# Kernel optimization log

Measured on AMD Instinct MI355X. Metric: run time of the kernel, lower is better.

## Reference

```python
import jax, jax.numpy as jnp
import numpy as np

D_MODEL = 1024
HEADS = 16
D_K = D_MODEL // HEADS
NEG_INF = -1e10


def setup_inputs() -> dict:
    key = jax.random.key(0)
    ks = jax.random.split(key, 10)
    n, s = 2, 2048
    inp = {
        "value": jax.random.normal(ks[0], (n, s, D_MODEL), dtype=jnp.float32),
        "key": jax.random.normal(ks[1], (n, s, D_MODEL), dtype=jnp.float32),
        "query": jax.random.normal(ks[2], (n, s, D_MODEL), dtype=jnp.float32),
        "mask": jax.random.randint(ks[3], (n, 1, s, s), 0, 2, dtype=jnp.int32),
        # torch.nn.Linear weights are [out, in]; y = x @ W.T (+ b)
        "Wq": jax.random.normal(ks[4], (D_MODEL, D_MODEL), dtype=jnp.float32) * (D_MODEL ** -0.5),
        "Wk": jax.random.normal(ks[5], (D_MODEL, D_MODEL), dtype=jnp.float32) * (D_MODEL ** -0.5),
        "Wv": jax.random.normal(ks[6], (D_MODEL, D_MODEL), dtype=jnp.float32) * (D_MODEL ** -0.5),
        "Wo": jax.random.normal(ks[7], (D_MODEL, D_MODEL), dtype=jnp.float32) * (D_MODEL ** -0.5),
        "bo": jax.random.normal(ks[8], (D_MODEL,), dtype=jnp.float32) * 0.01,
    }
    return inp


def reference(value, key, query, mask, Wq, Wk, Wv, Wo, bo):
    n, q_len, _ = query.shape
    # projections (Linear, no bias): x @ W.T
    q = (query @ Wq.T).reshape(n, q_len, HEADS, D_K)
    k = (key @ Wk.T).reshape(n, key.shape[1], HEADS, D_K)
    v = (value @ Wv.T).reshape(n, value.shape[1], HEADS, D_K)
    scores = jnp.einsum('nqhd,nkhd->nhqk', q, k)  # [n,h,q,k]
    scores = jnp.where(mask == 0, jnp.float32(NEG_INF), scores)
    attn = jax.nn.softmax(scores / jnp.sqrt(jnp.float32(D_K)), axis=-1)
    out = jnp.einsum('nhql,nlhd->nqhd', attn, v).reshape(n, q_len, D_MODEL)
    return out @ Wo.T + bo
```

## Files before the change

### kernel.cpp

```cpp
#include <hip/hip_runtime.h>
#include <hip/hip_bf16.h>
#include <stdint.h>

#define SEQ     2048
#define NBATCH  2
#define DMODEL  1024
#define NH      16
#define DKH     64

typedef __bf16 bf16;
typedef __attribute__((ext_vector_type(8))) __bf16 bf16x8;
typedef __attribute__((ext_vector_type(4))) __bf16 bf16x4;
typedef __attribute__((ext_vector_type(4))) float  f32x4;

static __device__ __forceinline__ f32x4 mfma16(bf16x8 a, bf16x8 b, f32x4 c) {
    return __builtin_amdgcn_mfma_f32_16x16x32_bf16(a, b, c, 0, 0, 0);
}

typedef const __attribute__((address_space(1))) void* gas_cptr;
typedef __attribute__((address_space(3))) void*       las_ptr;
#define GLDS16(g, l) __builtin_amdgcn_global_load_lds((gas_cptr)(g), (las_ptr)(l), 16, 0, 0)

#define PL32SWAP(a, b) asm("v_permlane32_swap_b32 %0, %1" : "+v"(a), "+v"(b))
#define PL16SWAP(a, b) asm("v_permlane16_swap_b32 %0, %1" : "+v"(a), "+v"(b))

__global__ __launch_bounds__(256) void cvt_all_k(const float* __restrict__ q,
                                                 const float* __restrict__ k,
                                                 const float* __restrict__ v,
                                                 const float* __restrict__ wq,
                                                 const float* __restrict__ wk,
                                                 const float* __restrict__ wv,
                                                 const float* __restrict__ wo,
                                                 const int* __restrict__ mask,
                                                 bf16* __restrict__ qb, bf16* __restrict__ kb,
                                                 bf16* __restrict__ vb, bf16* __restrict__ wqb,
                                                 bf16* __restrict__ wkb, bf16* __restrict__ wvb,
                                                 bf16* __restrict__ wob,
                                                 unsigned long long* __restrict__ mbits) {
    if (blockIdx.y == 7) {
        const int nwords = NBATCH * SEQ * (SEQ / 64);
        int wave  = (blockIdx.x * blockDim.x + threadIdx.x) >> 6;
        int lane  = threadIdx.x & 63;
        int nwtot = (gridDim.x * blockDim.x) >> 6;
        for (int w = wave; w < nwords; w += nwtot) {
            int m = mask[(size_t)w * 64 + lane];
            unsigned long long b = __ballot(m != 0);
            if (lane == 0) mbits[w] = b;
        }
        return;
    }
    const float* src; bf16* dst; int n4;
    const int NX4 = (NBATCH * SEQ * DMODEL) / 4, NW4 = (DMODEL * DMODEL) / 4;
    switch (blockIdx.y) {
        case 0: src = q;  dst = qb;  n4 = NX4; break;
        case 1: src = k;  dst = kb;  n4 = NX4; break;
        case 2: src = v;  dst = vb;  n4 = NX4; break;
        case 3: src = wq; dst = wqb; n4 = NW4; break;
        case 4: src = wk; dst = wkb; n4 = NW4; break;
        case 5: src = wv; dst = wvb; n4 = NW4; break;
        default: src = wo; dst = wob; n4 = NW4; break;
    }
    int stride = gridDim.x * blockDim.x;
    for (int i = blockIdx.x * blockDim.x + threadIdx.x; i < n4; i += stride) {
        f32x4 f = ((const f32x4*)src)[i];
        bf16x4 o;
#pragma unroll
        for (int j = 0; j < 4; j++) o[j] = (bf16)f[j];
        ((bf16x4*)dst)[i] = o;
    }
}

__global__ __launch_bounds__(256) void qkv_gemm(const bf16* __restrict__ Xq,
                                                const bf16* __restrict__ Xk,
                                                const bf16* __restrict__ Xv,
                                                const bf16* __restrict__ Wq,
                                                const bf16* __restrict__ Wk,
                                                const bf16* __restrict__ Wv,
                                                bf16* __restrict__ Qo,
                                                bf16* __restrict__ Ko,
                                                bf16* __restrict__ Vto) {
    __shared__ bf16 As[128 * 32], Bs[128 * 32];
    const int z = blockIdx.z;
    const bf16* A = (z == 0) ? Xq : (z == 1) ? Xk : Xv;
    const bf16* W = (z == 0) ? Wq : (z == 1) ? Wk : Wv;
    const int bm = blockIdx.x * 128, bn = blockIdx.y * 128;
    const int tid = threadIdx.x, wave = tid >> 6, lane = tid & 63;
    const int wm = wave >> 1, wn = wave & 1, lo = lane & 15, hi = lane >> 4;

    const int r0 = wave * 32 + (lane >> 2);
    const int c8 = (lane & 3) * 8;
    const bf16* Ag = A + (size_t)(bm + r0) * DMODEL + c8;
    const bf16* Bg = W + (size_t)(bn + r0) * DMODEL + c8;
    bf16* lA = &As[wave * 1024];
    bf16* lB = &Bs[wave * 1024];

    f32x4 acc[4][4];
#pragma unroll
    for (int i = 0; i < 4; i++)
#pragma unroll
        for (int j = 0; j < 4; j++) acc[i][j] = 0.0f;

    for (int k0 = 0; k0 < DMODEL; k0 += 32) {
        __syncthreads();
        GLDS16(Ag + k0, lA);
        GLDS16(Ag + k0 + (size_t)16 * DMODEL, lA + 512);
        GLDS16(Bg + k0, lB);
        GLDS16(Bg + k0 + (size_t)16 * DMODEL, lB + 512);
        __syncthreads();

        bf16x8 a[4], b[4];
#pragma unroll
        for (int t = 0; t < 4; t++) {
            a[t] = *(const bf16x8*)&As[(wm * 64 + t * 16 + lo) * 32 + hi * 8];
            b[t] = *(const bf16x8*)&Bs[(wn * 64 + t * 16 + lo) * 32 + hi * 8];
        }
#pragma unroll
        for (int tm = 0; tm < 4; tm++)
#pragma unroll
            for (int tn = 0; tn < 4; tn++)
                acc[tm][tn] = mfma16(a[tm], b[tn], acc[tm][tn]);
    }

    if (z < 2) {
        bf16* O = (z == 0) ? Qo : Ko;
        const float qscale = (z == 0) ? 0.18033688f : 1.0f;
#pragma unroll
        for (int tm = 0; tm < 4; tm++)
#pragma unroll
            for (int tn = 0; tn < 4; tn++)
#pragma unroll
                for (int r = 0; r < 4; r++) {
                    int m = bm + wm * 64 + tm * 16 + hi * 4 + r;
                    int o = bn + wn * 64 + tn * 16 + lo;
                    int nidx = m >> 11, sq = m & 2047;
                    int hh = o >> 6, d = o & 63;
                    O[(((size_t)nidx * NH + hh) * SEQ + sq) * DKH + d] = (bf16)(acc[tm][tn][r] * qscale);
                }
    } else {
#pragma unroll
        for (int tm = 0; tm < 4; tm++)
#pragma unroll
            for (int tn = 0; tn < 4; tn++)
#pragma unroll
                for (int r = 0; r < 4; r++) {
                    int m = bm + wm * 64 + tm * 16 + hi * 4 + r;
                    int o = bn + wn * 64 + tn * 16 + lo;
                    int nidx = m >> 11, sq = m & 2047;
                    int hh = o >> 6, d = o & 63;
                    Vto[(((size_t)nidx * NH + hh) * DKH + d) * SEQ + sq] = (bf16)acc[tm][tn][r];
                }
    }
}

__global__ __launch_bounds__(256, 8) void attn_k(const bf16* __restrict__ Q,
                                                 const bf16* __restrict__ K,
                                                 const bf16* __restrict__ Vt,
                                                 const unsigned long long* __restrict__ mbits,
                                                 bf16* __restrict__ Op0,
                                                 bf16* __restrict__ Op1,
                                                 float* __restrict__ Lp) {
    __shared__ bf16 Ks[64 * 72];
    __shared__ bf16 Vs[64 * 72];

    const int bid = blockIdx.x;
    const int xcd = bid & 7, j = bid >> 3;
    const int hd = xcd * 4 + (j & 3);
    const int qb = (j >> 2) & 31;
    const int ks = j >> 7;
    const int n = hd >> 4, h = hd & 15;

    const int tid = threadIdx.x, wave = tid >> 6, lane = tid & 63;
    const int lo = lane & 15, hi = lane >> 4;

    const size_t headoff = (size_t)hd * SEQ * DKH;
    const bf16* Qh = Q + headoff;
    const bf16* Kh = K + headoff;
    const bf16* Vh = Vt + headoff;

    const int qrow = qb * 64 + wave * 16 + lo;
    const bf16x8 aq0 = *(const bf16x8*)(Qh + (size_t)qrow * DKH + hi * 8);
    const bf16x8 aq1 = *(const bf16x8*)(Qh + (size_t)qrow * DKH + 32 + hi * 8);

    bf16x8 ones;
#pragma unroll
    for (int i = 0; i < 8; i++) ones[i] = (bf16)1.0f;

    f32x4 oacc[4];
#pragma unroll
    for (int t = 0; t < 4; t++) oacc[t] = 0.0f;
    f32x4 lacc; lacc = 0.0f;

    const unsigned long long* mbq = mbits + ((size_t)n * SEQ + qrow) * (SEQ / 64);

    const int kbeg = ks * 1024, kend = kbeg + 1024;

    const int srow = tid >> 3, sseg = tid & 7;
    const bf16* Kg = Kh + (size_t)srow * DKH + sseg * 8;
    const bf16* Vg = Vh + (size_t)srow * SEQ + sseg * 8;

    bf16x8 rk0 = *(const bf16x8*)(Kg + (size_t)kbeg * DKH);
    bf16x8 rk1 = *(const bf16x8*)(Kg + (size_t)(kbeg + 32) * DKH);
    bf16x8 rv0 = *(const bf16x8*)(Vg + kbeg);
    bf16x8 rv1 = *(const bf16x8*)(Vg + (size_t)32 * SEQ + kbeg);
    unsigned long long wm = mbq[kbeg >> 6];
    unsigned long long wmn = 0;

#pragma unroll 1
    for (int k0 = kbeg; k0 < kend; k0 += 64) {
        __syncthreads();
        *(bf16x8*)&Ks[srow * 72 + sseg * 8]        = rk0;
        *(bf16x8*)&Ks[(srow + 32) * 72 + sseg * 8] = rk1;
        *(bf16x8*)&Vs[srow * 72 + sseg * 8]        = rv0;
        *(bf16x8*)&Vs[(srow + 32) * 72 + sseg * 8] = rv1;
        if (k0 + 64 < kend) {
            rk0 = *(const bf16x8*)(Kg + (size_t)(k0 + 64) * DKH);
            rk1 = *(const bf16x8*)(Kg + (size_t)(k0 + 96) * DKH);
            rv0 = *(const bf16x8*)(Vg + k0 + 64);
            rv1 = *(const bf16x8*)(Vg + (size_t)32 * SEQ + k0 + 64);
            wmn = mbq[(k0 >> 6) + 1];
        }
        __syncthreads();

        unsigned wlo = (unsigned)(wm >> (hi * 4));
        unsigned whi = (unsigned)(wm >> (hi * 4 + 32));
        uint32_t pk[4][2];
#pragma unroll
        for (int tn = 0; tn < 4; tn++) {
            const int kr = (tn * 16 + lo) * 72;
            bf16x8 b0 = *(const bf16x8*)&Ks[kr + hi * 8];
            bf16x8 b1 = *(const bf16x8*)&Ks[kr + 32 + hi * 8];
            f32x4 z4; z4 = 0.0f;
            z4 = mfma16(b0, aq0, z4);
            z4 = mfma16(b1, aq1, z4);
            unsigned ws = ((tn < 2) ? wlo : whi) >> ((tn & 1) * 16);
            float pv[4];
#pragma unroll
            for (int r = 0; r < 4; r++) {
                float e = __builtin_amdgcn_exp2f(z4[r]);
                pv[r] = ((ws >> r) & 1u) ? e : 0.0f;
            }
            asm("v_cvt_pk_bf16_f32 %0, %1, %2" : "=v"(pk[tn][0]) : "v"(pv[0]), "v"(pv[1]));
            asm("v_cvt_pk_bf16_f32 %0, %1, %2" : "=v"(pk[tn][1]) : "v"(pv[2]), "v"(pv[3]));
        }
        wm = wmn;

        uint32_t d00 = pk[0][0], d02 = pk[1][0];
        PL32SWAP(d00, d02); PL16SWAP(d00, d02);
        uint32_t d01 = pk[0][1], d03 = pk[1][1];
        PL32SWAP(d01, d03); PL16SWAP(d01, d03);
        uint32_t d10 = pk[2][0], d12 = pk[3][0];
        PL32SWAP(d10, d12); PL16SWAP(d10, d12);
        uint32_t d11 = pk[2][1], d13 = pk[3][1];
        PL32SWAP(d11, d13); PL16SWAP(d11, d13);

        union FragU { uint32_t u[4]; bf16x8 v; };
        FragU f0, f1;
        f0.u[0] = d00; f0.u[1] = d01; f0.u[2] = d02; f0.u[3] = d03;
        f1.u[0] = d10; f1.u[1] = d11; f1.u[2] = d12; f1.u[3] = d13;
        bf16x8 ap0 = f0.v;
        bf16x8 ap1 = f1.v;

#pragma unroll
        for (int td = 0; td < 4; td++) {
            bf16x8 b0 = *(const bf16x8*)&Vs[(td * 16 + lo) * 72 + hi * 8];
            bf16x8 b1 = *(const bf16x8*)&Vs[(td * 16 + lo) * 72 + 32 + hi * 8];
            oacc[td] = mfma16(ap0, b0, oacc[td]);
            oacc[td] = mfma16(ap1, b1, oacc[td]);
        }
        lacc = mfma16(ap0, ones, lacc);
        lacc = mfma16(ap1, ones, lacc);
    }

    bf16* Op = ks ? Op1 : Op0;
#pragma unroll
    for (int td = 0; td < 4; td++)
#pragma unroll
        for (int r = 0; r < 4; r++) {
            int q = qb * 64 + wave * 16 + hi * 4 + r;
            int d = td * 16 + lo;
            Op[((size_t)n * SEQ + q) * DMODEL + h * 64 + d] = (bf16)oacc[td][r];
        }
    if (lo == 0) {
#pragma unroll
        for (int r = 0; r < 4; r++) {
            int q = qb * 64 + wave * 16 + hi * 4 + r;
            Lp[(size_t)ks * (NBATCH * NH * SEQ) + ((size_t)(n * NH + h) * SEQ) + q] = lacc[r];
        }
    }
}

__global__ __launch_bounds__(256) void merge_k(const bf16* __restrict__ o0,
                                               const bf16* __restrict__ o1,
                                               const float* __restrict__ lp,
                                               bf16* __restrict__ Aout) {
    int t = blockIdx.x * blockDim.x + threadIdx.x;
    int q = t >> 7;
    int h = (t >> 3) & 15;
    int n = q >> 11;
    bf16x8 a = ((const bf16x8*)o0)[t];
    bf16x8 b = ((const bf16x8*)o1)[t];
    int li = (n * NH + h) * SEQ + (q & 2047);
    float l = lp[li] + lp[NBATCH * NH * SEQ + li];
    float rl = 1.0f / l;
    bf16x8 o;
#pragma unroll
    for (int i = 0; i < 8; i++) o[i] = (bf16)(((float)a[i] + (float)b[i]) * rl);
    ((bf16x8*)Aout)[t] = o;
}

__global__ __launch_bounds__(256) void out_gemm(const bf16* __restrict__ A,
                                                const bf16* __restrict__ W,
                                                const float* __restrict__ bias,
                                                float* __restrict__ Out) {
    __shared__ bf16 As[128 * 32], Bs[128 * 32];
    const int bm = blockIdx.x * 128, bn = blockIdx.y * 128;
    const int tid = threadIdx.x, wave = tid >> 6, lane = tid & 63;
    const int wm = wave >> 1, wn = wave & 1, lo = lane & 15, hi = lane >> 4;

    const int r0 = wave * 32 + (lane >> 2);
    const int c8 = (lane & 3) * 8;
    const bf16* Ag = A + (size_t)(bm + r0) * DMODEL + c8;
    const bf16* Bg = W + (size_t)(bn + r0) * DMODEL + c8;
    bf16* lA = &As[wave * 1024];
    bf16* lB = &Bs[wave * 1024];

    f32x4 acc[4][4];
#pragma unroll
    for (int i = 0; i < 4; i++)
#pragma unroll
        for (int j = 0; j < 4; j++) acc[i][j] = 0.0f;

    for (int k0 = 0; k0 < DMODEL; k0 += 32) {
        __syncthreads();
        GLDS16(Ag + k0, lA);
        GLDS16(Ag + k0 + (size_t)16 * DMODEL, lA + 512);
        GLDS16(Bg + k0, lB);
        GLDS16(Bg + k0 + (size_t)16 * DMODEL, lB + 512);
        __syncthreads();

        bf16x8 a[4], b[4];
#pragma unroll
        for (int t = 0; t < 4; t++) {
            a[t] = *(const bf16x8*)&As[(wm * 64 + t * 16 + lo) * 32 + hi * 8];
            b[t] = *(const bf16x8*)&Bs[(wn * 64 + t * 16 + lo) * 32 + hi * 8];
        }
#pragma unroll
        for (int tm = 0; tm < 4; tm++)
#pragma unroll
            for (int tn = 0; tn < 4; tn++)
                acc[tm][tn] = mfma16(a[tm], b[tn], acc[tm][tn]);
    }

#pragma unroll
    for (int tm = 0; tm < 4; tm++)
#pragma unroll
        for (int tn = 0; tn < 4; tn++) {
            int o = bn + wn * 64 + tn * 16 + lo;
            float bv = bias[o];
#pragma unroll
            for (int r = 0; r < 4; r++) {
                int m = bm + wm * 64 + tm * 16 + hi * 4 + r;
                Out[(size_t)m * DMODEL + o] = acc[tm][tn][r] + bv;
            }
        }
}

extern "C" void kernel_launch(void* const* d_in, const int* in_sizes, int n_in,
                              void* d_out, int out_size, void* d_ws, size_t ws_size,
                              hipStream_t stream) {
    const float* value = (const float*)d_in[0];
    const float* key   = (const float*)d_in[1];
    const float* query = (const float*)d_in[2];
    const int*   mask  = (const int*)d_in[3];
    const float* Wq    = (const float*)d_in[4];
    const float* Wk    = (const float*)d_in[5];
    const float* Wv    = (const float*)d_in[6];
    const float* Wo    = (const float*)d_in[7];
    const float* bo    = (const float*)d_in[8];
    float* out = (float*)d_out;

    char* ws = (char*)d_ws;
    bf16* Qws = (bf16*)(ws);
    bf16* Kws = (bf16*)(ws + (8u  << 20));
    bf16* Vt  = (bf16*)(ws + (16u << 20));
    bf16* Xqb = (bf16*)(ws + (24u << 20));
    bf16* Xkb = (bf16*)(ws + (32u << 20));
    bf16* Xvb = (bf16*)(ws + (40u << 20));
    bf16* Wqb = (bf16*)(ws + (48u << 20));
    bf16* Wkb = (bf16*)(ws + (50u << 20));
    bf16* Wvb = (bf16*)(ws + (52u << 20));
    bf16* Wob = (bf16*)(ws + (54u << 20));
    unsigned long long* mbits = (unsigned long long*)(ws + (56u << 20));
    bf16*  Op0 = Xqb;
    bf16*  Op1 = Xkb;
    bf16*  Aws = Xvb;
    float* Lp  = (float*)Wqb;

    cvt_all_k<<<dim3(1024, 8), 256, 0, stream>>>(query, key, value, Wq, Wk, Wv, Wo, mask,
                                                 Xqb, Xkb, Xvb, Wqb, Wkb, Wvb, Wob, mbits);
    qkv_gemm<<<dim3(32, 8, 3), 256, 0, stream>>>(Xqb, Xkb, Xvb, Wqb, Wkb, Wvb, Qws, Kws, Vt);
    attn_k<<<2048, 256, 0, stream>>>(Qws, Kws, Vt, mbits, Op0, Op1, Lp);
    merge_k<<<2048, 256, 0, stream>>>(Op0, Op1, Lp, Aws);
    out_gemm<<<dim3(32, 8), 256, 0, stream>>>(Aws, Wob, bo, out);
}
```

Measured before the change: 331.0 us.

## Process two query tiles per attention block to reuse staged K/V tiles

Each attention block now handles 128 query rows (two 64-row sub-tiles) instead of 64, so every K/V tile staged in shared memory feeds twice as many MFMAs. The grid is halved to 1024 blocks and the occupancy hint drops from 8 to 4 blocks per CU to make room for the doubled accumulators and Q fragments. This cuts global K/V traffic and per-tile sync overhead, at the cost of higher register pressure and fewer resident waves to hide latency.

```diff
diff --git a/kernel.cpp b/kernel.cpp
--- a/kernel.cpp
+++ b/kernel.cpp
@@ -152,7 +152,7 @@
     }
 }
 
-__global__ __launch_bounds__(256, 8) void attn_k(const bf16* __restrict__ Q,
+__global__ __launch_bounds__(256, 4) void attn_k(const bf16* __restrict__ Q,
                                                  const bf16* __restrict__ K,
                                                  const bf16* __restrict__ Vt,
                                                  const unsigned long long* __restrict__ mbits,
@@ -165,8 +165,8 @@
     const int bid = blockIdx.x;
     const int xcd = bid & 7, j = bid >> 3;
     const int hd = xcd * 4 + (j & 3);
-    const int qb = (j >> 2) & 31;
-    const int ks = j >> 7;
+    const int qb = (j >> 2) & 15;
+    const int ks = j >> 6;
     const int n = hd >> 4, h = hd & 15;
 
     const int tid = threadIdx.x, wave = tid >> 6, lane = tid & 63;
@@ -177,20 +177,25 @@
     const bf16* Kh = K + headoff;
     const bf16* Vh = Vt + headoff;
 
-    const int qrow = qb * 64 + wave * 16 + lo;
-    const bf16x8 aq0 = *(const bf16x8*)(Qh + (size_t)qrow * DKH + hi * 8);
-    const bf16x8 aq1 = *(const bf16x8*)(Qh + (size_t)qrow * DKH + 32 + hi * 8);
+    const int qrowA = qb * 128 + wave * 16 + lo;
+    const int qrowB = qrowA + 64;
+    const bf16x8 aq0A = *(const bf16x8*)(Qh + (size_t)qrowA * DKH + hi * 8);
+    const bf16x8 aq1A = *(const bf16x8*)(Qh + (size_t)qrowA * DKH + 32 + hi * 8);
+    const bf16x8 aq0B = *(const bf16x8*)(Qh + (size_t)qrowB * DKH + hi * 8);
+    const bf16x8 aq1B = *(const bf16x8*)(Qh + (size_t)qrowB * DKH + 32 + hi * 8);
 
     bf16x8 ones;
 #pragma unroll
     for (int i = 0; i < 8; i++) ones[i] = (bf16)1.0f;
 
-    f32x4 oacc[4];
-#pragma unroll
-    for (int t = 0; t < 4; t++) oacc[t] = 0.0f;
-    f32x4 lacc; lacc = 0.0f;
-
-    const unsigned long long* mbq = mbits + ((size_t)n * SEQ + qrow) * (SEQ / 64);
+    f32x4 oaccA[4], oaccB[4];
+#pragma unroll
+    for (int t = 0; t < 4; t++) { oaccA[t] = 0.0f; oaccB[t] = 0.0f; }
+    f32x4 laccA; laccA = 0.0f;
+    f32x4 laccB; laccB = 0.0f;
+
+    const unsigned long long* mbqA = mbits + ((size_t)n * SEQ + qrowA) * (SEQ / 64);
+    const unsigned long long* mbqB = mbits + ((size_t)n * SEQ + qrowB) * (SEQ / 64);
 
     const int kbeg = ks * 1024, kend = kbeg + 1024;
 
@@ -202,8 +207,11 @@
     bf16x8 rk1 = *(const bf16x8*)(Kg + (size_t)(kbeg + 32) * DKH);
     bf16x8 rv0 = *(const bf16x8*)(Vg + kbeg);
     bf16x8 rv1 = *(const bf16x8*)(Vg + (size_t)32 * SEQ + kbeg);
-    unsigned long long wm = mbq[kbeg >> 6];
-    unsigned long long wmn = 0;
+    unsigned long long wmA = mbqA[kbeg >> 6];
+    unsigned long long wmB = mbqB[kbeg >> 6];
+    unsigned long long wmnA = 0, wmnB = 0;
+
+    union FragU { uint32_t u[4]; bf16x8 v; };
 
 #pragma unroll 1
     for (int k0 = kbeg; k0 < kend; k0 += 64) {
@@ -217,58 +225,88 @@
             rk1 = *(const bf16x8*)(Kg + (size_t)(k0 + 96) * DKH);
             rv0 = *(const bf16x8*)(Vg + k0 + 64);
             rv1 = *(const bf16x8*)(Vg + (size_t)32 * SEQ + k0 + 64);
-            wmn = mbq[(k0 >> 6) + 1];
-        }
-        __syncthreads();
-
-        unsigned wlo = (unsigned)(wm >> (hi * 4));
-        unsigned whi = (unsigned)(wm >> (hi * 4 + 32));
-        uint32_t pk[4][2];
+            wmnA = mbqA[(k0 >> 6) + 1];
+            wmnB = mbqB[(k0 >> 6) + 1];
+        }
+        __syncthreads();
+
+        unsigned wloA = (unsigned)(wmA >> (hi * 4));
+        unsigned whiA = (unsigned)(wmA >> (hi * 4 + 32));
+        unsigned wloB = (unsigned)(wmB >> (hi * 4));
+        unsigned whiB = (unsigned)(wmB >> (hi * 4 + 32));
+        uint32_t pkA[4][2], pkB[4][2];
 #pragma unroll
         for (int tn = 0; tn < 4; tn++) {
             const int kr = (tn * 16 + lo) * 72;
             bf16x8 b0 = *(const bf16x8*)&Ks[kr + hi * 8];
             bf16x8 b1 = *(const bf16x8*)&Ks[kr + 32 + hi * 8];
-            f32x4 z4; z4 = 0.0f;
-            z4 = mfma16(b0, aq0, z4);
-            z4 = mfma16(b1, aq1, z4);
-            unsigned ws = ((tn < 2) ? wlo : whi) >> ((tn & 1) * 16);
-            float pv[4];
+            f32x4 zA; zA = 0.0f;
+            zA = mfma16(b0, aq0A, zA);
+            zA = mfma16(b1, aq1A, zA);
+            f32x4 zB; zB = 0.0f;
+            zB = mfma16(b0, aq0B, zB);
+            zB = mfma16(b1, aq1B, zB);
+            unsigned wsA = ((tn < 2) ? wloA : whiA) >> ((tn & 1) * 16);
+            unsigned wsB = ((tn < 2) ? wloB : whiB) >> ((tn & 1) * 16);
+            float pvA[4], pvB[4];
 #pragma unroll
             for (int r = 0; r < 4; r++) {
-                float e = __builtin_amdgcn_exp2f(z4[r]);
-                pv[r] = ((ws >> r) & 1u) ? e : 0.0f;
+                float eA = __builtin_amdgcn_exp2f(zA[r]);
+                pvA[r] = ((wsA >> r) & 1u) ? eA : 0.0f;
+                float eB = __builtin_amdgcn_exp2f(zB[r]);
+                pvB[r] = ((wsB >> r) & 1u) ? eB : 0.0f;
             }
-            asm("v_cvt_pk_bf16_f32 %0, %1, %2" : "=v"(pk[tn][0]) : "v"(pv[0]), "v"(pv[1]));
-            asm("v_cvt_pk_bf16_f32 %0, %1, %2" : "=v"(pk[tn][1]) : "v"(pv[2]), "v"(pv[3]));
-        }
-        wm = wmn;
-
-        uint32_t d00 = pk[0][0], d02 = pk[1][0];
-        PL32SWAP(d00, d02); PL16SWAP(d00, d02);
-        uint32_t d01 = pk[0][1], d03 = pk[1][1];
-        PL32SWAP(d01, d03); PL16SWAP(d01, d03);
-        uint32_t d10 = pk[2][0], d12 = pk[3][0];
-        PL32SWAP(d10, d12); PL16SWAP(d10, d12);
-        uint32_t d11 = pk[2][1], d13 = pk[3][1];
-        PL32SWAP(d11, d13); PL16SWAP(d11, d13);
-
-        union FragU { uint32_t u[4]; bf16x8 v; };
-        FragU f0, f1;
-        f0.u[0] = d00; f0.u[1] = d01; f0.u[2] = d02; f0.u[3] = d03;
-        f1.u[0] = d10; f1.u[1] = d11; f1.u[2] = d12; f1.u[3] = d13;
-        bf16x8 ap0 = f0.v;
-        bf16x8 ap1 = f1.v;
+            asm("v_cvt_pk_bf16_f32 %0, %1, %2" : "=v"(pkA[tn][0]) : "v"(pvA[0]), "v"(pvA[1]));
+            asm("v_cvt_pk_bf16_f32 %0, %1, %2" : "=v"(pkA[tn][1]) : "v"(pvA[2]), "v"(pvA[3]));
+            asm("v_cvt_pk_bf16_f32 %0, %1, %2" : "=v"(pkB[tn][0]) : "v"(pvB[0]), "v"(pvB[1]));
+            asm("v_cvt_pk_bf16_f32 %0, %1, %2" : "=v"(pkB[tn][1]) : "v"(pvB[2]), "v"(pvB[3]));
+        }
+        wmA = wmnA;
+        wmB = wmnB;
+
+        bf16x8 ap0A, ap1A, ap0B, ap1B;
+        {
+            uint32_t d00 = pkA[0][0], d02 = pkA[1][0];
+            PL32SWAP(d00, d02); PL16SWAP(d00, d02);
+            uint32_t d01 = pkA[0][1], d03 = pkA[1][1];
+            PL32SWAP(d01, d03); PL16SWAP(d01, d03);
+            uint32_t d10 = pkA[2][0], d12 = pkA[3][0];
+            PL32SWAP(d10, d12); PL16SWAP(d10, d12);
+            uint32_t d11 = pkA[2][1], d13 = pkA[3][1];
+            PL32SWAP(d11, d13); PL16SWAP(d11, d13);
+            FragU f0, f1;
+            f0.u[0] = d00; f0.u[1] = d01; f0.u[2] = d02; f0.u[3] = d03;
+            f1.u[0] = d10; f1.u[1] = d11; f1.u[2] = d12; f1.u[3] = d13;
+            ap0A = f0.v; ap1A = f1.v;
+        }
+        {
+            uint32_t d00 = pkB[0][0], d02 = pkB[1][0];
+            PL32SWAP(d00, d02); PL16SWAP(d00, d02);
+            uint32_t d01 = pkB[0][1], d03 = pkB[1][1];
+            PL32SWAP(d01, d03); PL16SWAP(d01, d03);
+            uint32_t d10 = pkB[2][0], d12 = pkB[3][0];
+            PL32SWAP(d10, d12); PL16SWAP(d10, d12);
+            uint32_t d11 = pkB[2][1], d13 = pkB[3][1];
+            PL32SWAP(d11, d13); PL16SWAP(d11, d13);
+            FragU f0, f1;
+            f0.u[0] = d00; f0.u[1] = d01; f0.u[2] = d02; f0.u[3] = d03;
+            f1.u[0] = d10; f1.u[1] = d11; f1.u[2] = d12; f1.u[3] = d13;
+            ap0B = f0.v; ap1B = f1.v;
+        }
 
 #pragma unroll
         for (int td = 0; td < 4; td++) {
             bf16x8 b0 = *(const bf16x8*)&Vs[(td * 16 + lo) * 72 + hi * 8];
             bf16x8 b1 = *(const bf16x8*)&Vs[(td * 16 + lo) * 72 + 32 + hi * 8];
-            oacc[td] = mfma16(ap0, b0, oacc[td]);
-            oacc[td] = mfma16(ap1, b1, oacc[td]);
-        }
-        lacc = mfma16(ap0, ones, lacc);
-        lacc = mfma16(ap1, ones, lacc);
+            oaccA[td] = mfma16(ap0A, b0, oaccA[td]);
+            oaccA[td] = mfma16(ap1A, b1, oaccA[td]);
+            oaccB[td] = mfma16(ap0B, b0, oaccB[td]);
+            oaccB[td] = mfma16(ap1B, b1, oaccB[td]);
+        }
+        laccA = mfma16(ap0A, ones, laccA);
+        laccA = mfma16(ap1A, ones, laccA);
+        laccB = mfma16(ap0B, ones, laccB);
+        laccB = mfma16(ap1B, ones, laccB);
     }
 
     bf16* Op = ks ? Op1 : Op0;
@@ -276,15 +314,20 @@
     for (int td = 0; td < 4; td++)
 #pragma unroll
         for (int r = 0; r < 4; r++) {
-            int q = qb * 64 + wave * 16 + hi * 4 + r;
+            int qA = qb * 128 + wave * 16 + hi * 4 + r;
+            int qB = qA + 64;
             int d = td * 16 + lo;
-            Op[((size_t)n * SEQ + q) * DMODEL + h * 64 + d] = (bf16)oacc[td][r];
+            Op[((size_t)n * SEQ + qA) * DMODEL + h * 64 + d] = (bf16)oaccA[td][r];
+            Op[((size_t)n * SEQ + qB) * DMODEL + h * 64 + d] = (bf16)oaccB[td][r];
         }
     if (lo == 0) {
 #pragma unroll
         for (int r = 0; r < 4; r++) {
-            int q = qb * 64 + wave * 16 + hi * 4 + r;
-            Lp[(size_t)ks * (NBATCH * NH * SEQ) + ((size_t)(n * NH + h) * SEQ) + q] = lacc[r];
+            int qA = qb * 128 + wave * 16 + hi * 4 + r;
+            int qB = qA + 64;
+            size_t base = (size_t)ks * (NBATCH * NH * SEQ) + ((size_t)(n * NH + h) * SEQ);
+            Lp[base + qA] = laccA[r];
+            Lp[base + qB] = laccB[r];
         }
     }
 }
@@ -399,7 +442,7 @@
     cvt_all_k<<<dim3(1024, 8), 256, 0, stream>>>(query, key, value, Wq, Wk, Wv, Wo, mask,
                                                  Xqb, Xkb, Xvb, Wqb, Wkb, Wvb, Wob, mbits);
     qkv_gemm<<<dim3(32, 8, 3), 256, 0, stream>>>(Xqb, Xkb, Xvb, Wqb, Wkb, Wvb, Qws, Kws, Vt);
-    attn_k<<<2048, 256, 0, stream>>>(Qws, Kws, Vt, mbits, Op0, Op1, Lp);
+    attn_k<<<1024, 256, 0, stream>>>(Qws, Kws, Vt, mbits, Op0, Op1, Lp);
     merge_k<<<2048, 256, 0, stream>>>(Op0, Op1, Lp, Aws);
     out_gemm<<<dim3(32, 8), 256, 0, stream>>>(Aws, Wob, bo, out);
 }
```

Result: faster. 272.6 us (-17.6%).
